# Optimization experiments

Measured on AMD Instinct MI355X. Metric: run time of the kernel, lower is better.

Reference implementation:

```python
import jax, jax.numpy as jnp
import numpy as np

TEMPERATURE = 0.5
MAX_VAL = 11  # indices < 3**10, so 3-adic valuation of |i-j| is <= 10


def _cdist(z):
    # Euclidean pairwise distance via gram trick (matches torch.cdist p=2)
    sq = jnp.sum(z * z, axis=1)  # [n]
    d2 = sq[:, None] + sq[None, :] - 2.0 * (z @ z.T)
    return jnp.sqrt(jnp.maximum(d2, 0.0))


def _padic_dist(indices):
    # 3-adic distance: 3^(-v3(|i-j|)), 0 on the diagonal / equal indices
    diff = jnp.abs(indices[:, None] - indices[None, :])  # [n, n] int
    k = jnp.zeros(diff.shape, dtype=jnp.int32)
    for t in range(1, MAX_VAL + 1):
        k = k + (diff % (3 ** t) == 0).astype(jnp.int32)
    pd = jnp.power(jnp.float32(3.0), -k.astype(jnp.float32))
    return jnp.where(diff == 0, 0.0, pd)


def setup_inputs() -> dict:
    key = jax.random.key(0)
    k1, k2 = jax.random.split(key)
    z = jax.random.normal(k1, (8192, 1024), dtype=jnp.float32)
    indices = jax.random.randint(k2, (8192,), 0, 59049, dtype=jnp.int64)
    return {"z": z, "indices": indices}


def reference(z, indices):
    n = z.shape[0]
    latent_dist = _cdist(z)                      # [n, n]
    padic_dist = _padic_dist(indices)            # [n, n]
    latent_ranks = jax.nn.softmax(-latent_dist / TEMPERATURE, axis=1)
    padic_ranks = jax.nn.softmax(-padic_dist / TEMPERATURE, axis=1)
    # F.kl_div(log_q, p, reduction='batchmean') = mean_i sum_j p*(log p - log q)
    log_q = jnp.log(latent_ranks)
    kl = jnp.sum(padic_ranks * (jnp.log(padic_ranks) - log_q)) / n
    return kl
```

## Files before the change

kernel.cpp:

```cpp
#include <hip/hip_runtime.h>
#include <hip/hip_bf16.h>
#include <math.h>

#define GLOBAL_AS __attribute__((address_space(1)))
#define LDS_AS __attribute__((address_space(3)))

typedef int i32x4 __attribute__((ext_vector_type(4)));

#define N 8192
#define D 1024
#define QSCALE 18.0f
#define INV_S2 (1.0f / (QSCALE * QSCALE))
#define HOFF1 0
#define HOFF2 3
#define HOFF3 12
#define HOFF4 39
#define HOFF5 120
#define HOFF6 363
#define HOFF7 1092
#define HOFF8 3279
#define HOFF9 9840
#define HOFF10 29523
#define HTOT 88572

#if __has_builtin(__builtin_amdgcn_sqrtf)
#define FSQRT(x) __builtin_amdgcn_sqrtf(x)
#else
#define FSQRT(x) sqrtf(x)
#endif

__global__ __launch_bounds__(256) void prep_kernel(
    const float* __restrict__ z, signed char* __restrict__ zq,
    float* __restrict__ sq, int* __restrict__ hist) {
  const int r = blockIdx.x, t = threadIdx.x;
  if (r < 346) {
    const int o = r * 256 + t;
    if (o < HTOT) hist[o] = 0;
  }
  const float4 v = *(const float4*)(z + (size_t)r * D + t * 4);
  float f[4] = {v.x, v.y, v.z, v.w};
  int qq[4];
  float s = 0.f;
#pragma unroll
  for (int u = 0; u < 4; ++u) {
    float x = f[u];
    s = fmaf(x, x, s);
    int q = (int)rintf(x * QSCALE);
    q = max(-127, min(127, q));
    qq[u] = q;
  }
  const unsigned packed = (unsigned)(qq[0] & 255) | ((unsigned)(qq[1] & 255) << 8) |
                          ((unsigned)(qq[2] & 255) << 16) | ((unsigned)(qq[3] & 255) << 24);
  *(unsigned*)(zq + (size_t)r * D + t * 4) = packed;
#pragma unroll
  for (int o = 32; o >= 1; o >>= 1) s += __shfl_down(s, o, 64);
  __shared__ float red[4];
  const int lane = t & 63, wv = t >> 6;
  if (lane == 0) red[wv] = s;
  __syncthreads();
  if (t == 0) sq[r] = ((red[0] + red[1]) + red[2]) + red[3];
}

__global__ __launch_bounds__(256) void hist_kernel(
    const int* __restrict__ idx, int* __restrict__ hist) {
  const unsigned mi = (unsigned)idx[blockIdx.x * 256 + threadIdx.x];
  atomicAdd(&hist[HOFF8 + (mi % 6561u)], 1);
  atomicAdd(&hist[HOFF10 + mi], 1);
}

__global__ __launch_bounds__(256) void fold_kernel(int* __restrict__ hist) {
  const int b = blockIdx.x, t = threadIdx.x;
  if (b < 77) {
    const int r = b * 256 + t;
    if (r < 19683)
      hist[HOFF9 + r] =
          hist[HOFF10 + r] + hist[HOFF10 + r + 19683] + hist[HOFF10 + r + 39366];
    return;
  }
  __shared__ int lh[3279];
  for (int r = t; r < 2187; r += 256)
    lh[r] = hist[HOFF8 + r] + hist[HOFF8 + r + 2187] + hist[HOFF8 + r + 4374];
  __syncthreads();
  for (int r = t; r < 729; r += 256) lh[2187 + r] = lh[r] + lh[r + 729] + lh[r + 1458];
  __syncthreads();
  for (int r = t; r < 243; r += 256)
    lh[2916 + r] = lh[2187 + r] + lh[2187 + r + 243] + lh[2187 + r + 486];
  __syncthreads();
  for (int r = t; r < 81; r += 256)
    lh[3159 + r] = lh[2916 + r] + lh[2916 + r + 81] + lh[2916 + r + 162];
  __syncthreads();
  for (int r = t; r < 27; r += 256)
    lh[3240 + r] = lh[3159 + r] + lh[3159 + r + 27] + lh[3159 + r + 54];
  __syncthreads();
  if (t < 9) lh[3267 + t] = lh[3240 + t] + lh[3240 + t + 9] + lh[3240 + t + 18];
  __syncthreads();
  if (t < 3) lh[3276 + t] = lh[3267 + t] + lh[3267 + t + 3] + lh[3267 + t + 6];
  __syncthreads();
  for (int r = t; r < 2187; r += 256) hist[HOFF7 + r] = lh[r];
  for (int r = t; r < 729; r += 256) hist[HOFF6 + r] = lh[2187 + r];
  for (int r = t; r < 243; r += 256) hist[HOFF5 + r] = lh[2916 + r];
  if (t < 81) hist[HOFF4 + t] = lh[3159 + t];
  if (t < 27) hist[HOFF3 + t] = lh[3240 + t];
  if (t < 9) hist[HOFF2 + t] = lh[3267 + t];
  if (t < 3) hist[HOFF1 + t] = lh[3276 + t];
}

__global__ __launch_bounds__(256, 3) void gram_kernel(
    const signed char* __restrict__ zq,
    const float* __restrict__ sq, const int* __restrict__ idx,
    float* __restrict__ Pws) {
  __shared__ __align__(16) signed char lds[2 * 128 * 128];
  __shared__ float lut12f[12];
  const int t = blockIdx.x;
  int ibv = (int)((sqrtf(8.f * (float)t + 1.f) - 1.f) * 0.5f);
  while ((ibv + 1) * (ibv + 2) / 2 <= t) ++ibv;
  while (ibv * (ibv + 1) / 2 > t) --ibv;
  const int ib = __builtin_amdgcn_readfirstlane(ibv);
  const int jb = __builtin_amdgcn_readfirstlane(t - ibv * (ibv + 1) / 2);

  const int tid = threadIdx.x;
  const int lane = tid & 63, wv = tid >> 6;
  const int wr = wv >> 1, wc = wv & 1;
  const int r0 = lane & 15, kg = lane >> 4;

  if (tid < 12) {
    const float Pl = (tid == 11) ? 0.f : -2.f * exp2f(-1.5849625007211562f * (float)tid);
    lut12f[tid] = exp2f(1.4426950408889634f * Pl);
  }

  const unsigned vbase =
      ((unsigned)(tid >> 3) * 1024u) + ((unsigned)((tid & 7) ^ ((tid >> 3) & 7)) * 16u);
  const char* aBase = (const char*)(zq + (size_t)ib * 128 * D) + vbase;
  const char* bBase = (const char*)(zq + (size_t)jb * 128 * D) + vbase;
  char* ldsc = (char*)&lds[0];

  const int ub = kg ^ (r0 & 3);
  const int kcx = (r0 >> 2) & 1;
  const unsigned aoff0 = (unsigned)((wr * 64 + r0) * 128 + (kcx * 4 + ub) * 16);
  const unsigned boff0 = (unsigned)(16384 + (wc * 64 + r0) * 128 + (kcx * 4 + ub) * 16);

  i32x4 acc[4][4];
  const i32x4 vz = {0, 0, 0, 0};
#pragma unroll
  for (int m = 0; m < 4; ++m)
#pragma unroll
    for (int n = 0; n < 4; ++n) acc[m][n] = vz;

#pragma unroll 1
  for (int ks = 0; ks < 8; ++ks) {
    const char* aP = aBase + (unsigned)(ks * 128);
    const char* bP = bBase + (unsigned)(ks * 128);
    char* ldA = ldsc + tid * 16;
    char* ldB = ldsc + 16384 + tid * 16;
    __syncthreads();
#pragma unroll 1
    for (int i4 = 0; i4 < 4; ++i4) {
      __builtin_amdgcn_global_load_lds((const GLOBAL_AS void*)aP,
                                       (LDS_AS void*)ldA, 16, 0, 0);
      aP += 32768; ldA += 4096;
    }
#pragma unroll 1
    for (int i4 = 0; i4 < 4; ++i4) {
      __builtin_amdgcn_global_load_lds((const GLOBAL_AS void*)bP,
                                       (LDS_AS void*)ldB, 16, 0, 0);
      bP += 32768; ldB += 4096;
    }
    __syncthreads();

#pragma unroll
    for (int kc = 0; kc < 2; ++kc) {
      const unsigned ax = aoff0 ^ (unsigned)(kc * 64);
      const unsigned bx = boff0 ^ (unsigned)(kc * 64);
      i32x4 a[4], b[4];
#pragma unroll
      for (int m = 0; m < 4; ++m) a[m] = *(const i32x4*)(ldsc + ax + m * 2048);
#pragma unroll
      for (int n = 0; n < 4; ++n) b[n] = *(const i32x4*)(ldsc + bx + n * 2048);
#pragma unroll
      for (int m = 0; m < 4; ++m)
#pragma unroll
        for (int n = 0; n < 4; ++n)
          acc[m][n] = __builtin_amdgcn_mfma_i32_16x16x64_i8(a[m], b[n], acc[m][n], 0, 0, 0);
    }
  }

  const int ibase = ib * 128 + wr * 64 + kg * 4;
  const int jbase = jb * 128 + wc * 64 + r0;
  float sqj[4];
  int idxj[4];
#pragma unroll
  for (int n = 0; n < 4; ++n) {
    sqj[n] = sq[jbase + n * 16];
    idxj[n] = idx[jbase + n * 16];
  }
  const int dslot = jb * 2 + wc;
  float cws[4] = {0.f, 0.f, 0.f, 0.f};
#pragma unroll
  for (int m = 0; m < 4; ++m) {
#pragma unroll
    for (int q = 0; q < 4; ++q) {
      const int i = ibase + m * 16 + q;
      const float sqi = sq[i];
      const int idxi = idx[i];
      float ws = 0.f;
#pragma unroll
      for (int n = 0; n < 4; ++n) {
        const int j = jbase + n * 16;
        const float g = (float)acc[m][n][q] * INV_S2;
        const float d2 = sqi + sqj[n] - 2.f * g;
        const float dd = FSQRT(fmaxf(d2, 0.f));
        const int di = idxi - idxj[n];
        const unsigned diff = (unsigned)(di < 0 ? -di : di);
        unsigned dq = diff, qq;
        int vvv = 0;
        qq = dq * 3534952507u; { const bool b = qq <= 17674762u;   dq = b ? qq : dq; vvv = b ? 5 : 0; }
        qq = dq * 1749801491u; { const bool b = qq <= 159072862u;  dq = b ? qq : dq; vvv += b ? 3 : 0; }
        qq = dq * 2863311531u; { const bool b = qq <= 1431655765u; dq = b ? qq : dq; vvv += b ? 1 : 0; }
        qq = dq * 2863311531u; { const bool b = qq <= 1431655765u; vvv += b ? 1 : 0; }
        vvv = (diff == 0u) ? 11 : vvv;
        const float w = lut12f[vvv];
        const float wdd = (i == j) ? 0.f : w * dd;
        ws += wdd;
        cws[n] += wdd;
      }
#pragma unroll
      for (int o = 1; o < 16; o <<= 1) ws += __shfl_xor(ws, o, 64);
      if (r0 == 0) Pws[(size_t)dslot * N + i] = ws;
    }
  }
  if (ib != jb) {
    const int tslot = ib * 2 + wr;
#pragma unroll
    for (int nn = 0; nn < 4; ++nn) {
      float a = cws[nn];
#pragma unroll
      for (int o = 16; o < 64; o <<= 1) a += __shfl_xor(a, o, 64);
      if (kg == 0) Pws[(size_t)tslot * N + jbase + nn * 16] = a;
    }
  }
}

__global__ __launch_bounds__(256) void r1_kernel(
    const float* __restrict__ Pws, const int* __restrict__ hist,
    const int* __restrict__ idx, float* __restrict__ t) {
  const int row = blockIdx.x * 256 + threadIdx.x;
  float ws = 0.f;
  for (int s = 0; s < 128; ++s) ws += Pws[(size_t)s * N + row];
  const unsigned mi = (unsigned)idx[row];
  int H[11];
  H[0] = N;
  H[1] = hist[HOFF1 + (mi % 3u)];
  H[2] = hist[HOFF2 + (mi % 9u)];
  H[3] = hist[HOFF3 + (mi % 27u)];
  H[4] = hist[HOFF4 + (mi % 81u)];
  H[5] = hist[HOFF5 + (mi % 243u)];
  H[6] = hist[HOFF6 + (mi % 729u)];
  H[7] = hist[HOFF7 + (mi % 2187u)];
  H[8] = hist[HOFF8 + (mi % 6561u)];
  H[9] = hist[HOFF9 + (mi % 19683u)];
  H[10] = hist[HOFF10 + mi];
  float Z = 0.f, PL = 0.f;
#pragma unroll
  for (int k = 0; k < 10; ++k) {
    const float pl = -2.f * exp2f(-1.5849625007211562f * (float)k);
    const float w = exp2f(1.4426950408889634f * pl);
    const float cnt = (float)(H[k] - H[k + 1]);
    Z = fmaf(cnt, w, Z);
    PL = fmaf(cnt, w * pl, PL);
  }
  Z += (float)H[10];
  t[row] = (PL + 2.f * ws) / Z - logf(Z);
}

__global__ __launch_bounds__(256) void r2_kernel(const float* __restrict__ t,
                                                 float* __restrict__ out) {
  __shared__ float red[256];
  float s = 0.f;
  for (int r = threadIdx.x; r < N; r += 256) s += t[r];
  red[threadIdx.x] = s;
  __syncthreads();
  for (int o = 128; o > 0; o >>= 1) {
    if (threadIdx.x < (unsigned)o) red[threadIdx.x] += red[threadIdx.x + o];
    __syncthreads();
  }
  if (threadIdx.x == 0) out[0] = red[0] / (float)N;
}

extern "C" void kernel_launch(void* const* d_in, const int* in_sizes, int n_in,
                              void* d_out, int out_size, void* d_ws, size_t ws_size,
                              hipStream_t stream) {
  const float* z = (const float*)d_in[0];
  const int* idx = (const int*)d_in[1];
  float* out = (float*)d_out;
  char* ws = (char*)d_ws;
  signed char* zq = (signed char*)ws;
  float* sq = (float*)(ws + ((size_t)32 << 20));
  float* Pws = (float*)(ws + ((size_t)32 << 20) + ((size_t)64 << 10));
  int* hist = (int*)(Pws + (size_t)128 * N);
  float* tt = (float*)(hist + HTOT);

  prep_kernel<<<N, 256, 0, stream>>>(z, zq, sq, hist);
  hist_kernel<<<32, 256, 0, stream>>>(idx, hist);
  fold_kernel<<<78, 256, 0, stream>>>(hist);
  gram_kernel<<<64 * 65 / 2, 256, 0, stream>>>(zq, sq, idx, Pws);
  r1_kernel<<<32, 256, 0, stream>>>(Pws, hist, idx, tt);
  r2_kernel<<<1, 256, 0, stream>>>(tt, out);
}
```

Baseline: 107.8 us.

## Double-buffer LDS tiles in gram kernel and use mod-243 weight table

Doubles the LDS staging buffer so the next K-slice is fetched with global_load_lds while MFMAs run on the current one, using explicit vmcnt waits and raw barriers in place of the two syncthreads per step. It also swaps the chained multiply-inverse 3-adic valuation for a lookup on diff mod 243, with a rare slow path when the remainder is zero. LDS use doubles and launch bounds drop from 3 to 2 blocks per CU, trading occupancy for overlap.

Result: slower. 123.0 us (+14.0%).

```diff
diff --git a/kernel.cpp b/kernel.cpp
--- a/kernel.cpp
+++ b/kernel.cpp
@@ -105,11 +105,12 @@
   if (t < 3) hist[HOFF1 + t] = lh[3276 + t];
 }
 
-__global__ __launch_bounds__(256, 3) void gram_kernel(
+__global__ __launch_bounds__(256, 2) void gram_kernel(
     const signed char* __restrict__ zq,
     const float* __restrict__ sq, const int* __restrict__ idx,
     float* __restrict__ Pws) {
-  __shared__ __align__(16) signed char lds[2 * 128 * 128];
+  __shared__ __align__(16) signed char lds[2 * 2 * 128 * 128];
+  __shared__ float w243f[244];
   __shared__ float lut12f[12];
   const int t = blockIdx.x;
   int ibv = (int)((sqrtf(8.f * (float)t + 1.f) - 1.f) * 0.5f);
@@ -127,6 +128,13 @@
     const float Pl = (tid == 11) ? 0.f : -2.f * exp2f(-1.5849625007211562f * (float)tid);
     lut12f[tid] = exp2f(1.4426950408889634f * Pl);
   }
+  if (tid < 243) {
+    int rr = tid, v = 0;
+    if (rr > 0) {
+      while (rr % 3 == 0) { rr /= 3; ++v; }
+    }
+    w243f[tid] = exp2f(1.4426950408889634f * (-2.f * exp2f(-1.5849625007211562f * (float)v)));
+  }
 
   const unsigned vbase =
       ((unsigned)(tid >> 3) * 1024u) + ((unsigned)((tid & 7) ^ ((tid >> 3) & 7)) * 16u);
@@ -146,13 +154,11 @@
 #pragma unroll
     for (int n = 0; n < 4; ++n) acc[m][n] = vz;
 
-#pragma unroll 1
-  for (int ks = 0; ks < 8; ++ks) {
+  auto STAGE = [&](int ks, int buf) __attribute__((always_inline)) {
     const char* aP = aBase + (unsigned)(ks * 128);
     const char* bP = bBase + (unsigned)(ks * 128);
-    char* ldA = ldsc + tid * 16;
-    char* ldB = ldsc + 16384 + tid * 16;
-    __syncthreads();
+    char* ldA = ldsc + buf * 32768 + tid * 16;
+    char* ldB = ldsc + buf * 32768 + 16384 + tid * 16;
 #pragma unroll 1
     for (int i4 = 0; i4 < 4; ++i4) {
       __builtin_amdgcn_global_load_lds((const GLOBAL_AS void*)aP,
@@ -165,23 +171,37 @@
                                        (LDS_AS void*)ldB, 16, 0, 0);
       bP += 32768; ldB += 4096;
     }
-    __syncthreads();
-
+  };
+
+  STAGE(0, 0);
+#pragma unroll 1
+  for (int ks = 0; ks < 8; ++ks) {
+    const int cur = ks & 1;
+    if (ks < 7) {
+      STAGE(ks + 1, cur ^ 1);
+      asm volatile("s_waitcnt vmcnt(8)" ::: "memory");
+    } else {
+      asm volatile("s_waitcnt vmcnt(0)" ::: "memory");
+    }
+    __builtin_amdgcn_s_barrier();
+
+    const char* bufc = ldsc + cur * 32768;
 #pragma unroll
     for (int kc = 0; kc < 2; ++kc) {
       const unsigned ax = aoff0 ^ (unsigned)(kc * 64);
       const unsigned bx = boff0 ^ (unsigned)(kc * 64);
       i32x4 a[4], b[4];
 #pragma unroll
-      for (int m = 0; m < 4; ++m) a[m] = *(const i32x4*)(ldsc + ax + m * 2048);
-#pragma unroll
-      for (int n = 0; n < 4; ++n) b[n] = *(const i32x4*)(ldsc + bx + n * 2048);
+      for (int m = 0; m < 4; ++m) a[m] = *(const i32x4*)(bufc + ax + m * 2048);
+#pragma unroll
+      for (int n = 0; n < 4; ++n) b[n] = *(const i32x4*)(bufc + bx + n * 2048);
 #pragma unroll
       for (int m = 0; m < 4; ++m)
 #pragma unroll
         for (int n = 0; n < 4; ++n)
           acc[m][n] = __builtin_amdgcn_mfma_i32_16x16x64_i8(a[m], b[n], acc[m][n], 0, 0, 0);
     }
+    __builtin_amdgcn_s_barrier();
   }
 
   const int ibase = ib * 128 + wr * 64 + kg * 4;
@@ -211,14 +231,22 @@
         const float dd = FSQRT(fmaxf(d2, 0.f));
         const int di = idxi - idxj[n];
         const unsigned diff = (unsigned)(di < 0 ? -di : di);
-        unsigned dq = diff, qq;
-        int vvv = 0;
-        qq = dq * 3534952507u; { const bool b = qq <= 17674762u;   dq = b ? qq : dq; vvv = b ? 5 : 0; }
-        qq = dq * 1749801491u; { const bool b = qq <= 159072862u;  dq = b ? qq : dq; vvv += b ? 3 : 0; }
-        qq = dq * 2863311531u; { const bool b = qq <= 1431655765u; dq = b ? qq : dq; vvv += b ? 1 : 0; }
-        qq = dq * 2863311531u; { const bool b = qq <= 1431655765u; vvv += b ? 1 : 0; }
-        vvv = (diff == 0u) ? 11 : vvv;
-        const float w = lut12f[vvv];
+        const unsigned qd = __umulhi(diff, 17674763u);
+        const unsigned rm = diff - qd * 243u;
+        float w = w243f[rm];
+        if (__builtin_expect(rm == 0u, 0)) {
+          int vvv;
+          if (diff == 0u) {
+            vvv = 11;
+          } else {
+            unsigned q2 = qd, t2;
+            vvv = 5;
+            t2 = q2 * 1749801491u; if (t2 <= 159072862u)  { q2 = t2; vvv += 3; }
+            t2 = q2 * 2863311531u; if (t2 <= 1431655765u) { q2 = t2; vvv += 1; }
+            t2 = q2 * 2863311531u; if (t2 <= 1431655765u) { vvv += 1; }
+          }
+          w = lut12f[vvv];
+        }
         const float wdd = (i == j) ? 0.f : w * dd;
         ws += wdd;
         cws[n] += wdd;
```
